# Optimization experiments

Measured on AMD Instinct MI355X. Metric: run time of the kernel, lower is better.

The kernel has to match this reference:

```python
import jax, jax.numpy as jnp
import numpy as np
from jax import lax

LOG2PI = float(np.log(2.0 * np.pi))
N_K, N_T, N_C, N_D, N_SPK = 256, 128, 32, 10, 1000000

def _std_normal_logpdf(x):
    return -0.5 * (x * x + LOG2PI)

def _normal_logpdf(x, mu, log_sig):
    z = (x - mu) * jnp.exp(-log_sig)
    return -0.5 * (z * z + LOG2PI) - log_sig

def safe_log(x, minval=1e-10):
    return jnp.log(x + minval)

def setup_inputs() -> dict:
    key = jax.random.key(0)
    ks_ = jax.random.split(key, 8)
    s = jax.random.normal(ks_[0], (N_SPK, N_D), dtype=jnp.float32)
    y = jax.random.normal(ks_[1], (N_K, N_T), dtype=jnp.float32)
    ks = jax.random.randint(ks_[2], (N_SPK,), 0, N_K, dtype=jnp.int32)
    ts = jax.random.randint(ks_[3], (N_SPK,), 0, N_T, dtype=jnp.int32)
    means = jax.random.normal(ks_[4], (N_C, N_D), dtype=jnp.float32)
    A = jax.random.normal(ks_[5], (N_C, N_D, N_D), dtype=jnp.float32)
    covs = jnp.einsum('cij,ckj->cik', A, A) / N_D + jnp.eye(N_D, dtype=jnp.float32)
    b_mu = jax.random.normal(ks_[6], (N_C,), dtype=jnp.float32)
    b_log_sig = jax.random.normal(ks_[7], (N_C,), dtype=jnp.float32)
    beta_mu = jax.random.normal(jax.random.fold_in(key, 10), (N_C, N_T), dtype=jnp.float32)
    beta_log_sig = jax.random.normal(jax.random.fold_in(key, 11), (N_C, N_T), dtype=jnp.float32)
    return {"s": s, "y": y, "ks": ks, "ts": ts, "means": means, "covs": covs,
            "b_mu": b_mu, "b_log_sig": b_log_sig, "beta_mu": beta_mu, "beta_log_sig": beta_log_sig}

def _mvn_ll(s, means, covs):
    # ll[n, c] = MVN(means[c], covs[c]).log_prob(s[n]); loop over small n_c via lax.map
    L = jnp.linalg.cholesky(covs)                       # (c, d, d)
    logdet = 2.0 * jnp.sum(jnp.log(jnp.diagonal(L, axis1=1, axis2=2)), axis=1)  # (c,)
    d = s.shape[1]
    def comp(args):
        mu, Lc, ld = args
        diff = s - mu                                   # (n, d)
        z = jax.scipy.linalg.solve_triangular(Lc, diff.T, lower=True)  # (d, n)
        return -0.5 * (d * LOG2PI + ld + jnp.sum(z * z, axis=0))       # (n,)
    return lax.map(comp, (means, L, logdet)).T          # (n, c)

def reference(s, y, ks, ts, means, covs, b_mu, b_log_sig, beta_mu, beta_log_sig):
    # sampling=False path: use variational means
    b_sample, beta_sample = b_mu, beta_mu               # (c,), (c, t)
    # log_lambdas[k, c, t] = b[c] + beta[c, t] * y[k, t]
    log_lambdas = b_sample[None, :, None] + beta_sample[None, :, :] * y[:, None, :]
    log_pis = jax.nn.log_softmax(log_lambdas, axis=1)   # (k, c, t)
    ll = _mvn_ll(s, means, covs)                        # (n, c)
    logits = ll + log_pis[ks, :, ts]                    # per-spike gather -> (n, c)
    r = jax.nn.softmax(logits, axis=1)                  # responsibilities (n, c)
    log_prior = jnp.sum(_std_normal_logpdf(b_sample)) + jnp.sum(_std_normal_logpdf(beta_sample))
    log_q = jnp.sum(_normal_logpdf(b_sample, b_mu, b_log_sig)) + \
            jnp.sum(_normal_logpdf(beta_sample, beta_mu, beta_log_sig))
    elbo = log_prior - log_q
    elbo += jnp.sum(r * logits)
    elbo -= jnp.sum(r * safe_log(r))
    return elbo
```

## Files before the change

### kernel.cpp

```cpp
#include <hip/hip_runtime.h>
#include <hip/hip_bf16.h>
#include <hip/hip_fp16.h>
#include <math.h>

#define NK 256
#define NT 128
#define NC 32
#define ND 10
#define NSPK 1000000
#define LOG2PI 1.8378770664093453f
#define NWCHUNK (NSPK / 64)
#define GRID 1024
#define NWAVES (GRID * 4)
#define LSTR 33

typedef __attribute__((ext_vector_type(8))) short short8;
typedef __attribute__((ext_vector_type(4))) float floatx4;
typedef __attribute__((ext_vector_type(4))) int intx4;

union FragCvt { intx4 i; short8 s; };
union H2Cvt { int i; __half2 h; };


__device__ inline unsigned pack_bf16(float a, float b) {
  __hip_bfloat16 ha = __float2bfloat16(a), hb = __float2bfloat16(b);
  unsigned short ua, ub;
  __builtin_memcpy(&ua, &ha, 2);
  __builtin_memcpy(&ub, &hb, 2);
  return (unsigned)ua | ((unsigned)ub << 16);
}

__global__ void prep1_kernel(const float* __restrict__ means,
                             const float* __restrict__ covs,
                             const float* __restrict__ b_mu,
                             const float* __restrict__ b_ls,
                             const float* __restrict__ beta_mu,
                             const float* __restrict__ beta_ls,
                             int* __restrict__ wt,
                             float* __restrict__ cpack,
                             double* __restrict__ acc,
                             unsigned int* __restrict__ counter) {
  int blk = blockIdx.x;
  int tid = threadIdx.x;

  if (blk == 0) {
    int c = tid;
    if (c >= NC) return;

    float M[ND][ND];
    #pragma unroll
    for (int i = 0; i < ND; ++i)
      #pragma unroll
      for (int j = 0; j < ND; ++j)
        M[i][j] = covs[c * ND * ND + i * ND + j];

    float logdet = 0.f;
    #pragma unroll
    for (int j = 0; j < ND; ++j) {
      float d = M[j][j];
      #pragma unroll
      for (int k = 0; k < ND; ++k) if (k < j) d -= M[j][k] * M[j][k];
      float sq = sqrtf(d);
      M[j][j] = sq;
      logdet += 2.f * __logf(sq);
      float inv = 1.f / sq;
      #pragma unroll
      for (int i = 0; i < ND; ++i) {
        if (i > j) {
          float s2 = M[i][j];
          #pragma unroll
          for (int k = 0; k < ND; ++k) if (k < j) s2 -= M[i][k] * M[j][k];
          M[i][j] = s2 * inv;
        }
      }
    }

    #pragma unroll
    for (int j = 0; j < ND; ++j) {
      M[j][j] = 1.f / M[j][j];
      #pragma unroll
      for (int i = 0; i < ND; ++i) {
        if (i > j) {
          float s2 = 0.f;
          #pragma unroll
          for (int k = 0; k < ND; ++k) if (k >= j && k < i) s2 += M[i][k] * M[k][j];
          M[i][j] = -s2 / M[i][i];
        }
      }
    }

    float pd[ND];
    #pragma unroll
    for (int i = 0; i < ND; ++i) {
      #pragma unroll
      for (int jj = 0; jj < ND; ++jj) {
        if (jj >= i) {
          float s2 = 0.f;
          #pragma unroll
          for (int k = 0; k < ND; ++k) if (k >= jj) s2 += M[k][i] * M[k][jj];
          if (jj > i) M[i][jj] = s2;
          else pd[i] = s2;
        }
      }
    }

    float mu[ND], qv[ND];
    #pragma unroll
    for (int i = 0; i < ND; ++i) mu[i] = means[c * ND + i];
    float muPmu = 0.f;
    #pragma unroll
    for (int i = 0; i < ND; ++i) {
      float a2 = pd[i] * mu[i];
      #pragma unroll
      for (int j = 0; j < ND; ++j) {
        if (j < i) a2 += M[j][i] * mu[j];
        if (j > i) a2 += M[i][j] * mu[j];
      }
      qv[i] = a2;
      muPmu += mu[i] * a2;
    }
    float cst = -0.5f * ((float)ND * LOG2PI + logdet + muPmu);

    float wv[64];
    int p = 0;
    #pragma unroll
    for (int i = 0; i < ND; ++i)
      #pragma unroll
      for (int j = 0; j < ND; ++j)
        if (j >= i && !(i == 9 && j == 9))
          wv[p++] = (i == j) ? -0.5f * pd[i] : -M[i][j];
    #pragma unroll
    for (int i = 0; i < ND; ++i) wv[54 + i] = qv[i];

    #pragma unroll
    for (int j = 0; j < 32; ++j) {
      float a = wv[2 * j], b = wv[2 * j + 1];
      float ah = __bfloat162float(__float2bfloat16(a));
      float bh = __bfloat162float(__float2bfloat16(b));
      wt[c * 32 + j] = (int)pack_bf16(ah, bh);
      wt[(32 + c) * 32 + j] = (int)pack_bf16(a - ah, b - bh);
    }
    cpack[c] = cst;
    cpack[32 + c] = -0.5f * pd[9];

  } else {
    float local = 0.f;
    for (int i = tid; i < NC; i += 256)
      local += fmaf(-0.5f * b_mu[i], b_mu[i], b_ls[i]);
    for (int i = tid; i < NC * NT; i += 256)
      local += fmaf(-0.5f * beta_mu[i], beta_mu[i], beta_ls[i]);
    #pragma unroll
    for (int off = 32; off > 0; off >>= 1) local += __shfl_down(local, off);
    __shared__ float red[4];
    if ((tid & 63) == 0) red[tid >> 6] = local;
    __syncthreads();
    if (tid == 0) {
      acc[0] = (double)(red[0] + red[1] + red[2] + red[3]);
      counter[0] = 0u;
    }
  }
}

__global__ void prep2_kernel(const float* __restrict__ y,
                             const float* __restrict__ b_mu,
                             const float* __restrict__ beta_mu,
                             const float* __restrict__ cpack,
                             __half* __restrict__ pisT) {
  int id = blockIdx.x * 256 + threadIdx.x;
  int t = id & (NT - 1);
  float yv = y[id];
  float v[NC];
  float m = -1e30f;
  #pragma unroll
  for (int c = 0; c < NC; ++c) {
    v[c] = fmaf(beta_mu[c * NT + t], yv, b_mu[c]);
    m = fmaxf(m, v[c]);
  }
  float ssum = 0.f;
  #pragma unroll
  for (int c = 0; c < NC; ++c) ssum += __expf(v[c] - m);
  float lz = m + __logf(ssum);
  __half* outp = pisT + (size_t)id * NC;
  #pragma unroll
  for (int c = 0; c < NC; ++c) outp[c] = __float2half(v[c] - lz + cpack[c]);
}

__global__ void __launch_bounds__(256)
__attribute__((amdgpu_waves_per_eu(4, 4)))
spike_kernel(const float* __restrict__ s,
             const int* __restrict__ ks,
             const int* __restrict__ ts,
             const int* __restrict__ wt,
             const float* __restrict__ cpack,
             const __half* __restrict__ pisT,
             double* __restrict__ acc,
             unsigned int* __restrict__ counter,
             float* __restrict__ out) {
  __shared__ int lds[4 * 64 * LSTR];
  __shared__ float red[4];

  int tid = threadIdx.x;
  int wid = tid >> 6, L = tid & 63;
  int r = L & 15, q = L >> 4;
  int* ldsw = &lds[wid * 64 * LSTR];

  FragCvt wf[2][2][2];
  #pragma unroll
  for (int h = 0; h < 2; ++h)
    #pragma unroll
    for (int mt = 0; mt < 2; ++mt)
      #pragma unroll
      for (int kk = 0; kk < 2; ++kk)
        wf[h][mt][kk].i =
            *(const intx4*)&wt[(h * 32 + mt * 16 + r) * 32 + kk * 16 + q * 4];

  float w99v[NC];
  #pragma unroll
  for (int c = 0; c < NC; ++c) w99v[c] = cpack[32 + c];

  float lse_sum = 0.f;
  int g = blockIdx.x * 4 + wid;

  int c = g;
  float svc[ND];
  int kvc, tvc;
  {
    int n = c * 64 + L;
    const float2* srow = (const float2*)(s + (size_t)n * ND);
    #pragma unroll
    for (int i = 0; i < 5; ++i) {
      float2 v2 = srow[i];
      svc[2 * i] = v2.x;
      svc[2 * i + 1] = v2.y;
    }
    kvc = ks[n];
    tvc = ts[n];
  }

  while (c < NWCHUNK) {
    int ktc = kvc * NT + tvc;
    const intx4* lpp = (const intx4*)(pisT + (size_t)ktc * NC);
    intx4 lraw[4];
    #pragma unroll
    for (int i = 0; i < 4; ++i) lraw[i] = lpp[i];

    {
      int rb = L * LSTR;
      float f[8];
      int p = 0;
      #pragma unroll
      for (int i = 0; i < ND; ++i) {
        #pragma unroll
        for (int j = i; j < ND; ++j) {
          if (i == 9 && j == 9) continue;
          f[p & 7] = svc[i] * svc[j];
          if ((p & 7) == 7) {
            intx4 v;
            v.x = (int)pack_bf16(f[0], f[1]);
            v.y = (int)pack_bf16(f[2], f[3]);
            v.z = (int)pack_bf16(f[4], f[5]);
            v.w = (int)pack_bf16(f[6], f[7]);
            *(intx4*)&ldsw[rb + (p >> 3) * 4] = v;
          }
          ++p;
        }
      }
      #pragma unroll
      for (int i = 0; i < ND; ++i) {
        f[p & 7] = svc[i];
        if ((p & 7) == 7) {
          intx4 v;
          v.x = (int)pack_bf16(f[0], f[1]);
          v.y = (int)pack_bf16(f[2], f[3]);
          v.z = (int)pack_bf16(f[4], f[5]);
          v.w = (int)pack_bf16(f[6], f[7]);
          *(intx4*)&ldsw[rb + (p >> 3) * 4] = v;
        }
        ++p;
      }
    }

    int c2 = c + NWAVES;
    float svn[ND];
    int kvn, tvn;
    {
      int cc = c2 < NWCHUNK ? c2 : 0;
      int n2 = cc * 64 + L;
      const float2* srow = (const float2*)(s + (size_t)n2 * ND);
      #pragma unroll
      for (int i = 0; i < 5; ++i) {
        float2 v2 = srow[i];
        svn[2 * i] = v2.x;
        svn[2 * i + 1] = v2.y;
      }
      kvn = ks[n2];
      tvn = ts[n2];
    }

    floatx4 accf[2][4];
    #pragma unroll
    for (int mt = 0; mt < 2; ++mt)
      #pragma unroll
      for (int nt = 0; nt < 4; ++nt)
        accf[mt][nt] = (floatx4){0.f, 0.f, 0.f, 0.f};

    #pragma unroll
    for (int nt = 0; nt < 4; ++nt) {
      FragCvt b0, b1;
      b0.i = *(const intx4*)&ldsw[(nt * 16 + r) * LSTR + q * 4];
      b1.i = *(const intx4*)&ldsw[(nt * 16 + r) * LSTR + 16 + q * 4];
      #pragma unroll
      for (int mt = 0; mt < 2; ++mt) {
        accf[mt][nt] = __builtin_amdgcn_mfma_f32_16x16x32_bf16(
            wf[0][mt][0].s, b0.s, accf[mt][nt], 0, 0, 0);
        accf[mt][nt] = __builtin_amdgcn_mfma_f32_16x16x32_bf16(
            wf[1][mt][0].s, b0.s, accf[mt][nt], 0, 0, 0);
        accf[mt][nt] = __builtin_amdgcn_mfma_f32_16x16x32_bf16(
            wf[0][mt][1].s, b1.s, accf[mt][nt], 0, 0, 0);
        accf[mt][nt] = __builtin_amdgcn_mfma_f32_16x16x32_bf16(
            wf[1][mt][1].s, b1.s, accf[mt][nt], 0, 0, 0);
      }
    }

    #pragma unroll
    for (int nt = 0; nt < 4; ++nt)
      #pragma unroll
      for (int mt = 0; mt < 2; ++mt)
        *(floatx4*)&ldsw[(nt * 16 + r) * LSTR + mt * 16 + q * 4] = accf[mt][nt];

    {
      int rb = L * LSTR;
      float lg[NC];
      #pragma unroll
      for (int gch = 0; gch < 8; ++gch) {
        intx4 lv = *(const intx4*)&ldsw[rb + gch * 4];
        lg[4 * gch + 0] = __int_as_float(lv.x);
        lg[4 * gch + 1] = __int_as_float(lv.y);
        lg[4 * gch + 2] = __int_as_float(lv.z);
        lg[4 * gch + 3] = __int_as_float(lv.w);
      }
      float s9sq = svc[9] * svc[9];
      #pragma unroll
      for (int gg = 0; gg < 16; ++gg) {
        H2Cvt hc;
        hc.i = ((const int*)lraw)[gg];
        lg[2 * gg + 0] += __low2float(hc.h) + w99v[2 * gg + 0] * s9sq;
        lg[2 * gg + 1] += __high2float(hc.h) + w99v[2 * gg + 1] * s9sq;
      }

      float m = lg[0];
      #pragma unroll
      for (int cc = 1; cc < NC; ++cc) m = fmaxf(m, lg[cc]);
      float ssum = 0.f;
      #pragma unroll
      for (int cc = 0; cc < NC; ++cc) ssum += __expf(lg[cc] - m);
      lse_sum += m + __logf(ssum);
    }

    c = c2;
    kvc = kvn;
    tvc = tvn;
    #pragma unroll
    for (int i = 0; i < ND; ++i) svc[i] = svn[i];
  }

  #pragma unroll
  for (int off = 32; off > 0; off >>= 1) lse_sum += __shfl_down(lse_sum, off);
  if ((tid & 63) == 0) red[tid >> 6] = lse_sum;
  __syncthreads();
  if (tid == 0) {
    atomicAdd(acc, (double)(red[0] + red[1] + red[2] + red[3]));
    __threadfence();
    unsigned int old = atomicAdd(counter, 1u);
    if (old == GRID - 1) {
      __threadfence();
      double v = atomicAdd(acc, 0.0);
      out[0] = (float)v;
    }
  }
}

extern "C" void kernel_launch(void* const* d_in, const int* in_sizes, int n_in,
                              void* d_out, int out_size, void* d_ws, size_t ws_size,
                              hipStream_t stream) {
  const float* s       = (const float*)d_in[0];
  const float* y       = (const float*)d_in[1];
  const int*   ks      = (const int*)d_in[2];
  const int*   ts      = (const int*)d_in[3];
  const float* means   = (const float*)d_in[4];
  const float* covs    = (const float*)d_in[5];
  const float* b_mu    = (const float*)d_in[6];
  const float* b_ls    = (const float*)d_in[7];
  const float* beta_mu = (const float*)d_in[8];
  const float* beta_ls = (const float*)d_in[9];
  float* out = (float*)d_out;

  char* ws = (char*)d_ws;
  double* acc           = (double*)ws;
  unsigned int* counter = (unsigned int*)(ws + 8);
  float* cpack          = (float*)(ws + 64);
  int* wt               = (int*)(ws + 1024);
  __half* pisT          = (__half*)(ws + 16384);

  prep1_kernel<<<2, 256, 0, stream>>>(
      means, covs, b_mu, b_ls, beta_mu, beta_ls, wt, cpack, acc, counter);
  prep2_kernel<<<(NK * NT) / 256, 256, 0, stream>>>(
      y, b_mu, beta_mu, cpack, pisT);
  spike_kernel<<<GRID, 256, 0, stream>>>(
      s, ks, ts, wt, cpack, pisT, acc, counter, out);
}
```

Baseline: 168.8 us.

## Launch one wave per spike chunk and do softmax directly in MFMA layout

Replaces the persistent grid-stride loop (1024 blocks with register prefetch of the next chunk) with one wave per 64-spike chunk over a grid sized to the problem, and relaxes waves_per_eu so more waves can be resident. The logsumexp is now done on the MFMA accumulator fragments directly, using cross-lane xor shuffles for max and sum. This removes the LDS round trip of the logits, and the log-pi gather is done per fragment using kt indices staged in LDS. The intent is to hide latency through occupancy rather than software prefetch. The cost is extra shuffles and many more blocks, each doing a double atomic at the end.

```diff
diff --git a/kernel.cpp b/kernel.cpp
--- a/kernel.cpp
+++ b/kernel.cpp
@@ -10,16 +10,18 @@
 #define NSPK 1000000
 #define LOG2PI 1.8378770664093453f
 #define NWCHUNK (NSPK / 64)
-#define GRID 1024
-#define NWAVES (GRID * 4)
-#define LSTR 33
+#define SGRID ((NWCHUNK + 3) / 4)
+
+#define FSTR 36
+#define WAVE_LDS (64 * FSTR + 128)
 
 typedef __attribute__((ext_vector_type(8))) short short8;
 typedef __attribute__((ext_vector_type(4))) float floatx4;
 typedef __attribute__((ext_vector_type(4))) int intx4;
+typedef __attribute__((ext_vector_type(2))) int intx2;
 
 union FragCvt { intx4 i; short8 s; };
-union H2Cvt { int i; __half2 h; };
+union LpCvt { intx2 i2; __half2 h2[2]; };
 
 
 __device__ inline unsigned pack_bf16(float a, float b) {
@@ -186,7 +188,7 @@
 }
 
 __global__ void __launch_bounds__(256)
-__attribute__((amdgpu_waves_per_eu(4, 4)))
+__attribute__((amdgpu_waves_per_eu(4, 8)))
 spike_kernel(const float* __restrict__ s,
              const int* __restrict__ ks,
              const int* __restrict__ ts,
@@ -196,13 +198,17 @@
              double* __restrict__ acc,
              unsigned int* __restrict__ counter,
              float* __restrict__ out) {
-  __shared__ int lds[4 * 64 * LSTR];
+  __shared__ int lds[4 * WAVE_LDS];
   __shared__ float red[4];
 
   int tid = threadIdx.x;
   int wid = tid >> 6, L = tid & 63;
   int r = L & 15, q = L >> 4;
-  int* ldsw = &lds[wid * 64 * LSTR];
+  int* ldsw = &lds[wid * WAVE_LDS];
+  int* ldkt = ldsw + 64 * FSTR;
+
+  int g = blockIdx.x * 4 + wid;
+  bool active = g < NWCHUNK;
 
   FragCvt wf[2][2][2];
   #pragma unroll
@@ -214,38 +220,35 @@
         wf[h][mt][kk].i =
             *(const intx4*)&wt[(h * 32 + mt * 16 + r) * 32 + kk * 16 + q * 4];
 
-  float w99v[NC];
-  #pragma unroll
-  for (int c = 0; c < NC; ++c) w99v[c] = cpack[32 + c];
+  float4 w99f[2];
+  #pragma unroll
+  for (int mt = 0; mt < 2; ++mt)
+    w99f[mt] = *(const float4*)&cpack[32 + mt * 16 + q * 4];
 
   float lse_sum = 0.f;
-  int g = blockIdx.x * 4 + wid;
-
-  int c = g;
-  float svc[ND];
-  int kvc, tvc;
-  {
-    int n = c * 64 + L;
+
+  if (active) {
+    int n = g * 64 + L;
+
     const float2* srow = (const float2*)(s + (size_t)n * ND);
+    float sv[ND];
     #pragma unroll
     for (int i = 0; i < 5; ++i) {
       float2 v2 = srow[i];
-      svc[2 * i] = v2.x;
-      svc[2 * i + 1] = v2.y;
-    }
-    kvc = ks[n];
-    tvc = ts[n];
-  }
-
-  while (c < NWCHUNK) {
-    int ktc = kvc * NT + tvc;
-    const intx4* lpp = (const intx4*)(pisT + (size_t)ktc * NC);
-    intx4 lraw[4];
-    #pragma unroll
-    for (int i = 0; i < 4; ++i) lraw[i] = lpp[i];
+      sv[2 * i] = v2.x;
+      sv[2 * i + 1] = v2.y;
+    }
+    int kt = ks[n] * NT + ts[n];
 
     {
-      int rb = L * LSTR;
+      intx2 kp;
+      kp.x = kt;
+      kp.y = __float_as_int(sv[9] * sv[9]);
+      *(intx2*)&ldkt[L * 2] = kp;
+    }
+
+    {
+      int rb = L * FSTR;
       float f[8];
       int p = 0;
       #pragma unroll
@@ -253,7 +256,7 @@
         #pragma unroll
         for (int j = i; j < ND; ++j) {
           if (i == 9 && j == 9) continue;
-          f[p & 7] = svc[i] * svc[j];
+          f[p & 7] = sv[i] * sv[j];
           if ((p & 7) == 7) {
             intx4 v;
             v.x = (int)pack_bf16(f[0], f[1]);
@@ -267,7 +270,7 @@
       }
       #pragma unroll
       for (int i = 0; i < ND; ++i) {
-        f[p & 7] = svc[i];
+        f[p & 7] = sv[i];
         if ((p & 7) == 7) {
           intx4 v;
           v.x = (int)pack_bf16(f[0], f[1]);
@@ -280,22 +283,23 @@
       }
     }
 
-    int c2 = c + NWAVES;
-    float svn[ND];
-    int kvn, tvn;
-    {
-      int cc = c2 < NWCHUNK ? c2 : 0;
-      int n2 = cc * 64 + L;
-      const float2* srow = (const float2*)(s + (size_t)n2 * ND);
-      #pragma unroll
-      for (int i = 0; i < 5; ++i) {
-        float2 v2 = srow[i];
-        svn[2 * i] = v2.x;
-        svn[2 * i + 1] = v2.y;
-      }
-      kvn = ks[n2];
-      tvn = ts[n2];
-    }
+    int kt4[4];
+    float s9sq4[4];
+    #pragma unroll
+    for (int nt = 0; nt < 4; ++nt) {
+      intx2 kp = *(const intx2*)&ldkt[(nt * 16 + r) * 2];
+      kt4[nt] = kp.x;
+      s9sq4[nt] = __int_as_float(kp.y);
+    }
+
+    intx2 lraw[4][2];
+    const char* ptbase = (const char*)pisT;
+    #pragma unroll
+    for (int nt = 0; nt < 4; ++nt)
+      #pragma unroll
+      for (int mt = 0; mt < 2; ++mt)
+        lraw[nt][mt] = *(const intx2*)(ptbase + (size_t)kt4[nt] * 64 +
+                                       mt * 32 + q * 8);
 
     floatx4 accf[2][4];
     #pragma unroll
@@ -307,8 +311,8 @@
     #pragma unroll
     for (int nt = 0; nt < 4; ++nt) {
       FragCvt b0, b1;
-      b0.i = *(const intx4*)&ldsw[(nt * 16 + r) * LSTR + q * 4];
-      b1.i = *(const intx4*)&ldsw[(nt * 16 + r) * LSTR + 16 + q * 4];
+      b0.i = *(const intx4*)&ldsw[(nt * 16 + r) * FSTR + q * 4];
+      b1.i = *(const intx4*)&ldsw[(nt * 16 + r) * FSTR + 16 + q * 4];
       #pragma unroll
       for (int mt = 0; mt < 2; ++mt) {
         accf[mt][nt] = __builtin_amdgcn_mfma_f32_16x16x32_bf16(
@@ -323,45 +327,36 @@
     }
 
     #pragma unroll
-    for (int nt = 0; nt < 4; ++nt)
+    for (int nt = 0; nt < 4; ++nt) {
+      float lg[2][4];
+      #pragma unroll
+      for (int mt = 0; mt < 2; ++mt) {
+        LpCvt lc;
+        lc.i2 = lraw[nt][mt];
+        float lp0 = __low2float(lc.h2[0]), lp1 = __high2float(lc.h2[0]);
+        float lp2 = __low2float(lc.h2[1]), lp3 = __high2float(lc.h2[1]);
+        lg[mt][0] = accf[mt][nt][0] + lp0 + w99f[mt].x * s9sq4[nt];
+        lg[mt][1] = accf[mt][nt][1] + lp1 + w99f[mt].y * s9sq4[nt];
+        lg[mt][2] = accf[mt][nt][2] + lp2 + w99f[mt].z * s9sq4[nt];
+        lg[mt][3] = accf[mt][nt][3] + lp3 + w99f[mt].w * s9sq4[nt];
+      }
+      float m = lg[0][0];
       #pragma unroll
       for (int mt = 0; mt < 2; ++mt)
-        *(floatx4*)&ldsw[(nt * 16 + r) * LSTR + mt * 16 + q * 4] = accf[mt][nt];
-
-    {
-      int rb = L * LSTR;
-      float lg[NC];
-      #pragma unroll
-      for (int gch = 0; gch < 8; ++gch) {
-        intx4 lv = *(const intx4*)&ldsw[rb + gch * 4];
-        lg[4 * gch + 0] = __int_as_float(lv.x);
-        lg[4 * gch + 1] = __int_as_float(lv.y);
-        lg[4 * gch + 2] = __int_as_float(lv.z);
-        lg[4 * gch + 3] = __int_as_float(lv.w);
-      }
-      float s9sq = svc[9] * svc[9];
-      #pragma unroll
-      for (int gg = 0; gg < 16; ++gg) {
-        H2Cvt hc;
-        hc.i = ((const int*)lraw)[gg];
-        lg[2 * gg + 0] += __low2float(hc.h) + w99v[2 * gg + 0] * s9sq;
-        lg[2 * gg + 1] += __high2float(hc.h) + w99v[2 * gg + 1] * s9sq;
-      }
-
-      float m = lg[0];
-      #pragma unroll
-      for (int cc = 1; cc < NC; ++cc) m = fmaxf(m, lg[cc]);
+        #pragma unroll
+        for (int rr = 0; rr < 4; ++rr) m = fmaxf(m, lg[mt][rr]);
+      m = fmaxf(m, __shfl_xor(m, 16));
+      m = fmaxf(m, __shfl_xor(m, 32));
       float ssum = 0.f;
       #pragma unroll
-      for (int cc = 0; cc < NC; ++cc) ssum += __expf(lg[cc] - m);
-      lse_sum += m + __logf(ssum);
-    }
-
-    c = c2;
-    kvc = kvn;
-    tvc = tvn;
-    #pragma unroll
-    for (int i = 0; i < ND; ++i) svc[i] = svn[i];
+      for (int mt = 0; mt < 2; ++mt)
+        #pragma unroll
+        for (int rr = 0; rr < 4; ++rr) ssum += __expf(lg[mt][rr] - m);
+      ssum += __shfl_xor(ssum, 16);
+      ssum += __shfl_xor(ssum, 32);
+      float lse = m + __logf(ssum);
+      lse_sum += (q == 0) ? lse : 0.f;
+    }
   }
 
   #pragma unroll
@@ -372,7 +367,7 @@
     atomicAdd(acc, (double)(red[0] + red[1] + red[2] + red[3]));
     __threadfence();
     unsigned int old = atomicAdd(counter, 1u);
-    if (old == GRID - 1) {
+    if (old == SGRID - 1) {
       __threadfence();
       double v = atomicAdd(acc, 0.0);
       out[0] = (float)v;
@@ -406,6 +401,6 @@
       means, covs, b_mu, b_ls, beta_mu, beta_ls, wt, cpack, acc, counter);
   prep2_kernel<<<(NK * NT) / 256, 256, 0, stream>>>(
       y, b_mu, beta_mu, cpack, pisT);
-  spike_kernel<<<GRID, 256, 0, stream>>>(
+  spike_kernel<<<SGRID, 256, 0, stream>>>(
       s, ks, ts, wt, cpack, pisT, acc, counter, out);
 }
```

After: 219.5 us. 30.1% more time.
